# Kernel optimization log

Hardware: AMD Instinct MI355X
Metric: run time of the kernel (lower is better)

The kernel has to match this reference:

```python
import jax, jax.numpy as jnp
import numpy as np

E = 256   # in_features / embed_dim
O = 256   # out_features
H = 8     # n_heads
D = E // H  # head_dim
NEG = -1e9
SLOPE = 0.2  # leaky_relu negative slope


def setup_inputs() -> dict:
    key = jax.random.key(0)
    ks = jax.random.split(key, 9)
    B, N = 8, 1024
    x = jax.random.normal(ks[0], (B, N, E), dtype=jnp.float32)
    adj_matrix = jax.random.randint(ks[1], (N, N), 0, 2, dtype=jnp.int32)
    s = 1.0 / np.sqrt(E)
    w_in = jax.random.uniform(ks[2], (3 * E, E), jnp.float32, -s, s)   # packed q/k/v proj (torch in_proj_weight)
    b_in = jnp.zeros((3 * E,), jnp.float32)
    w_out = jax.random.uniform(ks[3], (E, E), jnp.float32, -s, s)      # MHA out_proj
    b_out = jnp.zeros((E,), jnp.float32)
    w_lin = jax.random.uniform(ks[4], (O, E), jnp.float32, -s, s)      # final nn.Linear
    b_lin = jax.random.uniform(ks[5], (O,), jnp.float32, -s, s)
    return {"x": x, "adj_matrix": adj_matrix, "w_in": w_in, "b_in": b_in,
            "w_out": w_out, "b_out": b_out, "w_lin": w_lin, "b_lin": b_lin}


def reference(x, adj_matrix, w_in, b_in, w_out, b_out, w_lin, b_lin):
    B, N, _ = x.shape
    scale = 1.0 / np.sqrt(D)
    qkv = x @ w_in.T + b_in                      # [B,N,3E]
    q, k, v = jnp.split(qkv, 3, axis=-1)
    q = q.reshape(B, N, H, D) * scale
    k = k.reshape(B, N, H, D)
    v = v.reshape(B, N, H, D)
    scores = jnp.einsum('bnhd,bmhd->bhnm', q, k)  # [B,H,N,N]
    allowed = (adj_matrix != 0)[None, None]       # mask True where adj==0 -> disallowed
    scores = jnp.where(allowed, scores, NEG)
    attn = jax.nn.softmax(scores, axis=-1)
    ctx = jnp.einsum('bhnm,bmhd->bnhd', attn, v).reshape(B, N, E)
    attended = ctx @ w_out.T + b_out              # MHA output (dropout is identity in eval)
    out = attended @ w_lin.T + b_lin
    return jnp.where(out >= 0, out, SLOPE * out)  # leaky_relu(0.2)
```

## Files before the change

### kernel.cpp

```cpp
#include <hip/hip_runtime.h>
#include <math.h>

#define EE 256
#define HH 8
#define DD 32
#define NB 8
#define NS 1024
#define SLOPE 0.2f

typedef float f32x4 __attribute__((ext_vector_type(4)));
typedef short short8 __attribute__((ext_vector_type(8)));

static __device__ __forceinline__ unsigned short f2b(float f) {
    unsigned int u = __float_as_uint(f);
    u = (u + 0x7FFFu + ((u >> 16) & 1u)) >> 16;
    return (unsigned short)u;
}

static __device__ __forceinline__ unsigned int cvtpk(float lo, float hi) {
    unsigned int r;
    asm("v_cvt_pk_bf16_f32 %0, %1, %2" : "=v"(r) : "v"(lo), "v"(hi));
    return r;
}

static __device__ __forceinline__ void gload_lds16(const void* g, void* l) {
    __builtin_amdgcn_global_load_lds(
        (const __attribute__((address_space(1))) unsigned int*)g,
        (__attribute__((address_space(3))) unsigned int*)l, 16, 0, 0);
}

__global__ __launch_bounds__(256) void cvt_w(
    const float* __restrict__ wi, const float* __restrict__ wo,
    const float* __restrict__ wl, unsigned short* __restrict__ wib,
    unsigned short* __restrict__ wob, unsigned short* __restrict__ wlb) {
    int t = blockIdx.x * 256 + threadIdx.x;
    const float* src; unsigned short* dst; int base;
    if (t < 24576)      { src = wi; dst = wib; base = t; }
    else if (t < 32768) { src = wo; dst = wob; base = t - 24576; }
    else                { src = wl; dst = wlb; base = t - 32768; }
    const float4* s = (const float4*)(src + (size_t)base * 8);
    float4 a = s[0], b = s[1];
    uint4 wv;
    wv.x = cvtpk(a.x, a.y); wv.y = cvtpk(a.z, a.w);
    wv.z = cvtpk(b.x, b.y); wv.w = cvtpk(b.z, b.w);
    *(uint4*)(dst + (size_t)base * 8) = wv;
}

__global__ __launch_bounds__(256) void adj_to_bits(const int* __restrict__ adj,
                                                   unsigned int* __restrict__ bits) {
    int t = blockIdx.x * 256 + threadIdx.x;
    int n = t >> 5, w = t & 31;
    const int* p = adj + (size_t)n * NS + w * 32;
    unsigned int word = 0;
#pragma unroll
    for (int i = 0; i < 32; i += 4) {
        int4 a = *(const int4*)(p + i);
        if (a.x) word |= 1u << i;
        if (a.y) word |= 1u << (i + 1);
        if (a.z) word |= 1u << (i + 2);
        if (a.w) word |= 1u << (i + 3);
    }
    bits[t] = word;
}

template<int MODE>
__global__ __launch_bounds__(256) void gemm_mfma(
    const unsigned short* __restrict__ A, const float* __restrict__ Af,
    const unsigned short* __restrict__ W,
    const float* __restrict__ bias, void* __restrict__ out,
    unsigned short* __restrict__ qb, unsigned short* __restrict__ kb,
    unsigned short* __restrict__ vtb, int Nout) {
    __shared__ __align__(16) unsigned short As[128 * 64];
    __shared__ __align__(16) unsigned short Bs[64 * 64];
    int tid = threadIdx.x, w = tid >> 6, lane = tid & 63;
    int lq = lane & 15, g = lane >> 4;
    int wr = w >> 1, wc = w & 1;
    int m0 = blockIdx.y * 128, n0 = blockIdx.x * 64;
    int r8 = lane >> 3, c8 = (lane & 7) * 8;
    f32x4 acc[4][2];
#pragma unroll
    for (int i = 0; i < 4; ++i)
#pragma unroll
        for (int j = 0; j < 2; ++j) acc[i][j] = (f32x4){0.f, 0.f, 0.f, 0.f};

    for (int k0 = 0; k0 < 256; k0 += 64) {
        __syncthreads();
        if (MODE == 2) {
#pragma unroll
            for (int u = 0; u < 4; ++u) {
                int idx = u * 256 + tid;
                int r = idx >> 3, cc = (idx & 7) * 8;
                const float* src = Af + (size_t)(m0 + r) * 256 + k0 + cc;
                float4 a = *(const float4*)src;
                float4 b = *(const float4*)(src + 4);
                uint4 wv;
                wv.x = cvtpk(a.x, a.y); wv.y = cvtpk(a.z, a.w);
                wv.z = cvtpk(b.x, b.y); wv.w = cvtpk(b.z, b.w);
                *(uint4*)(&As[r * 64 + cc]) = wv;
            }
        } else {
#pragma unroll
            for (int i = 0; i < 4; ++i)
                gload_lds16(A + (size_t)(m0 + w * 32 + i * 8 + r8) * 256 + k0 + c8,
                            &As[(w * 32 + i * 8) * 64]);
        }
#pragma unroll
        for (int i = 0; i < 2; ++i)
            gload_lds16(W + (size_t)(n0 + w * 16 + i * 8 + r8) * 256 + k0 + c8,
                        &Bs[(w * 16 + i * 8) * 64]);
        __syncthreads();
#pragma unroll
        for (int ks = 0; ks < 2; ++ks) {
            short8 af[4], bf[2];
#pragma unroll
            for (int mi = 0; mi < 4; ++mi)
                af[mi] = *(const short8*)(&As[(wr * 64 + mi * 16 + lq) * 64 + ks * 32 + g * 8]);
#pragma unroll
            for (int ni = 0; ni < 2; ++ni)
                bf[ni] = *(const short8*)(&Bs[(wc * 32 + ni * 16 + lq) * 64 + ks * 32 + g * 8]);
#pragma unroll
            for (int mi = 0; mi < 4; ++mi)
#pragma unroll
                for (int ni = 0; ni < 2; ++ni)
                    acc[mi][ni] = __builtin_amdgcn_mfma_f32_16x16x32_bf16(af[mi], bf[ni], acc[mi][ni], 0, 0, 0);
        }
    }
    const float scale = 0.17677669529663687f;
#pragma unroll
    for (int mi = 0; mi < 4; ++mi) {
#pragma unroll
        for (int reg = 0; reg < 4; ++reg) {
            int m = m0 + wr * 64 + mi * 16 + g * 4 + reg;
#pragma unroll
            for (int ni = 0; ni < 2; ++ni) {
                int n = n0 + wc * 32 + ni * 16 + lq;
                float v = acc[mi][ni][reg] + bias[n];
                if (MODE == 0) {
                    ((unsigned short*)out)[(size_t)m * Nout + n] = f2b(v);
                } else if (MODE == 1) {
                    v = v >= 0.f ? v : SLOPE * v;
                    ((float*)out)[(size_t)m * Nout + n] = v;
                } else {
                    int sec = n >> 8, cc = n & 255, h = cc >> 5, d = cc & 31;
                    int b = m >> 10, nr = m & (NS - 1);
                    if (sec == 0)
                        qb[((size_t)(b * HH + h) * NS + nr) * DD + d] = f2b(v * scale);
                    else if (sec == 1)
                        kb[((size_t)(b * HH + h) * NS + nr) * DD + d] = f2b(v);
                    else
                        vtb[((size_t)(b * HH + h) * DD + d) * NS + nr] = f2b(v);
                }
            }
        }
    }
}

__global__ __launch_bounds__(256) void attn_mfma(
    const unsigned short* __restrict__ q, const unsigned short* __restrict__ k,
    const unsigned short* __restrict__ vt, const unsigned int* __restrict__ adjbits,
    unsigned short* __restrict__ ctx) {
    __shared__ __align__(16) unsigned short Ks[128 * 40];
    __shared__ __align__(16) unsigned short Vs[32 * 136];
    __shared__ __align__(16) unsigned short Ps[4 * 16 * 136];
    int tid = threadIdx.x;
    int w = tid >> 6, lane = tid & 63;
    int lq = lane & 15, g = lane >> 4;
    int bh = blockIdx.y;
    int n0 = blockIdx.x * 64;
    int nq = n0 + w * 16 + lq;
    const unsigned short* qb = q + (size_t)bh * NS * DD;
    const unsigned short* kb = k + (size_t)bh * NS * DD;
    const unsigned short* vb = vt + (size_t)bh * DD * NS;
    short8 qfrag = *(const short8*)(qb + (size_t)nq * DD + g * 8);
    const unsigned int* abr = adjbits + (size_t)nq * 32;
    float ls[4] = {0.f, 0.f, 0.f, 0.f};
    f32x4 acc0 = {0.f, 0.f, 0.f, 0.f}, acc1 = {0.f, 0.f, 0.f, 0.f};
    unsigned short* Pw = Ps + w * 16 * 136;
    int kr = tid >> 1, kc = (tid & 1) * 16;
    int vd = tid >> 3, vc = (tid & 7) * 16;

    for (int m0 = 0; m0 < NS; m0 += 128) {
        __syncthreads();
        {
            const unsigned short* ksrc = kb + (size_t)(m0 + kr) * DD + kc;
            *(int4*)(&Ks[kr * 40 + kc])     = *(const int4*)(ksrc);
            *(int4*)(&Ks[kr * 40 + kc + 8]) = *(const int4*)(ksrc + 8);
            const unsigned short* vsrc = vb + (size_t)vd * NS + m0 + vc;
            *(int4*)(&Vs[vd * 136 + vc])     = *(const int4*)(vsrc);
            *(int4*)(&Vs[vd * 136 + vc + 8]) = *(const int4*)(vsrc + 8);
        }
        __syncthreads();

        const f32x4 z = {0.f, 0.f, 0.f, 0.f};
        f32x4 s[8];
#pragma unroll
        for (int t = 0; t < 8; ++t) {
            short8 kf = *(const short8*)(&Ks[(16 * t + lq) * 40 + g * 8]);
            s[t] = __builtin_amdgcn_mfma_f32_16x16x32_bf16(kf, qfrag, z, 0, 0, 0);
        }
        uint4 w4 = *(const uint4*)(abr + (m0 >> 5));
#pragma unroll
        for (int t = 0; t < 8; ++t) {
            unsigned int wd = (t < 2) ? w4.x : (t < 4) ? w4.y : (t < 6) ? w4.z : w4.w;
            unsigned int bits = wd >> (16 * (t & 1) + 4 * g);
            float p0 = ((bits >> 0) & 1u) ? __expf(s[t][0]) : 0.f;
            float p1 = ((bits >> 1) & 1u) ? __expf(s[t][1]) : 0.f;
            float p2 = ((bits >> 2) & 1u) ? __expf(s[t][2]) : 0.f;
            float p3 = ((bits >> 3) & 1u) ? __expf(s[t][3]) : 0.f;
            ls[0] += p0; ls[1] += p1; ls[2] += p2; ls[3] += p3;
            uint2 uu;
            uu.x = cvtpk(p0, p1);
            uu.y = cvtpk(p2, p3);
            *(uint2*)(&Pw[lq * 136 + 16 * t + 4 * g]) = uu;
        }
#pragma unroll
        for (int kh = 0; kh < 4; ++kh) {
            short8 pf = *(const short8*)(&Pw[lq * 136 + kh * 32 + g * 8]);
            short8 v0 = *(const short8*)(&Vs[lq * 136 + kh * 32 + g * 8]);
            short8 v1 = *(const short8*)(&Vs[(16 + lq) * 136 + kh * 32 + g * 8]);
            acc0 = __builtin_amdgcn_mfma_f32_16x16x32_bf16(pf, v0, acc0, 0, 0, 0);
            acc1 = __builtin_amdgcn_mfma_f32_16x16x32_bf16(pf, v1, acc1, 0, 0, 0);
        }
    }
    float rs = (ls[0] + ls[1]) + (ls[2] + ls[3]);
    rs += __shfl_xor(rs, 16);
    rs += __shfl_xor(rs, 32);
    int b = bh >> 3, h = bh & 7;
#pragma unroll
    for (int i = 0; i < 4; ++i) {
        int nrow = n0 + w * 16 + g * 4 + i;
        float inv = 1.f / __shfl(rs, g * 4 + i);
        unsigned short* dst = ctx + ((size_t)(b * NS + nrow)) * EE + h * DD;
        dst[lq] = f2b(acc0[i] * inv);
        dst[16 + lq] = f2b(acc1[i] * inv);
    }
}

extern "C" void kernel_launch(void* const* d_in, const int* in_sizes, int n_in,
                              void* d_out, int out_size, void* d_ws, size_t ws_size,
                              hipStream_t stream) {
    const float* x     = (const float*)d_in[0];
    const int*   adj   = (const int*)d_in[1];
    const float* w_in  = (const float*)d_in[2];
    const float* b_in  = (const float*)d_in[3];
    const float* w_out = (const float*)d_in[4];
    const float* b_out = (const float*)d_in[5];
    const float* w_lin = (const float*)d_in[6];
    const float* b_lin = (const float*)d_in[7];
    float* out = (float*)d_out;

    const size_t S = (size_t)NB * HH * NS * DD;
    unsigned short* qb   = (unsigned short*)d_ws;
    unsigned short* kb   = qb + S;
    unsigned short* vtb  = kb + S;
    unsigned short* ctxb = vtb + S;
    unsigned short* attb = ctxb + S;
    unsigned short* wib  = attb + S;
    unsigned short* wob  = wib + 768 * 256;
    unsigned short* wlb  = wob + 256 * 256;
    unsigned int* adjbits = (unsigned int*)(wlb + 256 * 256);

    dim3 blk(256);
    cvt_w<<<dim3(160), blk, 0, stream>>>(w_in, w_out, w_lin, wib, wob, wlb);
    adj_to_bits<<<dim3((NS * 32) / 256), blk, 0, stream>>>(adj, adjbits);
    gemm_mfma<2><<<dim3(12, 64), blk, 0, stream>>>(nullptr, x, wib, b_in, nullptr, qb, kb, vtb, 768);
    attn_mfma<<<dim3(NS / 64, NB * HH), blk, 0, stream>>>(qb, kb, vtb, adjbits, ctxb);
    gemm_mfma<0><<<dim3(4, 64), blk, 0, stream>>>(ctxb, nullptr, wob, b_out, attb, nullptr, nullptr, nullptr, 256);
    gemm_mfma<1><<<dim3(4, 64), blk, 0, stream>>>(attb, nullptr, wlb, b_lin, out, nullptr, nullptr, nullptr, 256);
}
```

Measured before the change: 79.14 us.

## Fold out_proj and final linear into one combined weight; pre-convert x to bf16

Precomputes W_lin·W_out and the combined bias on the device each call, so the two back-to-back linear layers become a single GEMM. This drops one GEMM launch and the bf16 round trip of the intermediate activations. The x-to-bf16 conversion also moves out of the QKV GEMM into its own pass, so that GEMM can use direct global-to-LDS loads. In exchange it adds a naive fp32 256x256x256 weight product kernel and extra launches, and rounds the combined weight to bf16.

```diff
diff --git a/kernel.cpp b/kernel.cpp
--- a/kernel.cpp
+++ b/kernel.cpp
@@ -29,21 +29,44 @@
         (__attribute__((address_space(3))) unsigned int*)l, 16, 0, 0);
 }
 
-__global__ __launch_bounds__(256) void cvt_w(
-    const float* __restrict__ wi, const float* __restrict__ wo,
-    const float* __restrict__ wl, unsigned short* __restrict__ wib,
-    unsigned short* __restrict__ wob, unsigned short* __restrict__ wlb) {
+__global__ __launch_bounds__(256) void cvt_x(const float* __restrict__ x,
+                                             unsigned short* __restrict__ xb) {
     int t = blockIdx.x * 256 + threadIdx.x;
-    const float* src; unsigned short* dst; int base;
-    if (t < 24576)      { src = wi; dst = wib; base = t; }
-    else if (t < 32768) { src = wo; dst = wob; base = t - 24576; }
-    else                { src = wl; dst = wlb; base = t - 32768; }
-    const float4* s = (const float4*)(src + (size_t)base * 8);
+    const float4* s = (const float4*)(x + (size_t)t * 8);
     float4 a = s[0], b = s[1];
     uint4 wv;
     wv.x = cvtpk(a.x, a.y); wv.y = cvtpk(a.z, a.w);
     wv.z = cvtpk(b.x, b.y); wv.w = cvtpk(b.z, b.w);
-    *(uint4*)(dst + (size_t)base * 8) = wv;
+    *(uint4*)(xb + (size_t)t * 8) = wv;
+}
+
+__global__ __launch_bounds__(256) void cvt_wi(const float* __restrict__ wi,
+                                              unsigned short* __restrict__ wib) {
+    int t = blockIdx.x * 256 + threadIdx.x;
+    const float4* s = (const float4*)(wi + (size_t)t * 8);
+    float4 a = s[0], b = s[1];
+    uint4 wv;
+    wv.x = cvtpk(a.x, a.y); wv.y = cvtpk(a.z, a.w);
+    wv.z = cvtpk(b.x, b.y); wv.w = cvtpk(b.z, b.w);
+    *(uint4*)(wib + (size_t)t * 8) = wv;
+}
+
+__global__ __launch_bounds__(256) void make_comb(
+    const float* __restrict__ wo, const float* __restrict__ bo,
+    const float* __restrict__ wl, const float* __restrict__ bl,
+    unsigned short* __restrict__ wcb, float* __restrict__ bcomb) {
+    int o = blockIdx.x, c = threadIdx.x;
+    const float* wlr = wl + (size_t)o * EE;
+    float acc = 0.f;
+#pragma unroll 8
+    for (int e = 0; e < EE; ++e)
+        acc = fmaf(wlr[e], wo[(size_t)e * EE + c], acc);
+    wcb[(size_t)o * EE + c] = f2b(acc);
+    if (c == 0) {
+        float bb = bl[o];
+        for (int e = 0; e < EE; ++e) bb = fmaf(wlr[e], bo[e], bb);
+        bcomb[o] = bb;
+    }
 }
 
 __global__ __launch_bounds__(256) void adj_to_bits(const int* __restrict__ adj,
@@ -65,8 +88,7 @@
 
 template<int MODE>
 __global__ __launch_bounds__(256) void gemm_mfma(
-    const unsigned short* __restrict__ A, const float* __restrict__ Af,
-    const unsigned short* __restrict__ W,
+    const unsigned short* __restrict__ A, const unsigned short* __restrict__ W,
     const float* __restrict__ bias, void* __restrict__ out,
     unsigned short* __restrict__ qb, unsigned short* __restrict__ kb,
     unsigned short* __restrict__ vtb, int Nout) {
@@ -85,25 +107,10 @@
 
     for (int k0 = 0; k0 < 256; k0 += 64) {
         __syncthreads();
-        if (MODE == 2) {
-#pragma unroll
-            for (int u = 0; u < 4; ++u) {
-                int idx = u * 256 + tid;
-                int r = idx >> 3, cc = (idx & 7) * 8;
-                const float* src = Af + (size_t)(m0 + r) * 256 + k0 + cc;
-                float4 a = *(const float4*)src;
-                float4 b = *(const float4*)(src + 4);
-                uint4 wv;
-                wv.x = cvtpk(a.x, a.y); wv.y = cvtpk(a.z, a.w);
-                wv.z = cvtpk(b.x, b.y); wv.w = cvtpk(b.z, b.w);
-                *(uint4*)(&As[r * 64 + cc]) = wv;
-            }
-        } else {
-#pragma unroll
-            for (int i = 0; i < 4; ++i)
-                gload_lds16(A + (size_t)(m0 + w * 32 + i * 8 + r8) * 256 + k0 + c8,
-                            &As[(w * 32 + i * 8) * 64]);
-        }
+#pragma unroll
+        for (int i = 0; i < 4; ++i)
+            gload_lds16(A + (size_t)(m0 + w * 32 + i * 8 + r8) * 256 + k0 + c8,
+                        &As[(w * 32 + i * 8) * 64]);
 #pragma unroll
         for (int i = 0; i < 2; ++i)
             gload_lds16(W + (size_t)(n0 + w * 16 + i * 8 + r8) * 256 + k0 + c8,
@@ -135,9 +142,7 @@
             for (int ni = 0; ni < 2; ++ni) {
                 int n = n0 + wc * 32 + ni * 16 + lq;
                 float v = acc[mi][ni][reg] + bias[n];
-                if (MODE == 0) {
-                    ((unsigned short*)out)[(size_t)m * Nout + n] = f2b(v);
-                } else if (MODE == 1) {
+                if (MODE == 1) {
                     v = v >= 0.f ? v : SLOPE * v;
                     ((float*)out)[(size_t)m * Nout + n] = v;
                 } else {
@@ -254,17 +259,18 @@
     unsigned short* kb   = qb + S;
     unsigned short* vtb  = kb + S;
     unsigned short* ctxb = vtb + S;
-    unsigned short* attb = ctxb + S;
-    unsigned short* wib  = attb + S;
-    unsigned short* wob  = wib + 768 * 256;
-    unsigned short* wlb  = wob + 256 * 256;
-    unsigned int* adjbits = (unsigned int*)(wlb + 256 * 256);
+    unsigned short* xb   = ctxb + S;
+    unsigned short* wib  = xb + S;
+    unsigned short* wcb  = wib + 768 * 256;
+    unsigned int* adjbits = (unsigned int*)(wcb + 256 * 256);
+    float* bcomb = (float*)(adjbits + 32768);
 
     dim3 blk(256);
-    cvt_w<<<dim3(160), blk, 0, stream>>>(w_in, w_out, w_lin, wib, wob, wlb);
+    cvt_x<<<dim3(1024), blk, 0, stream>>>(x, xb);
+    cvt_wi<<<dim3(96), blk, 0, stream>>>(w_in, wib);
+    make_comb<<<dim3(256), blk, 0, stream>>>(w_out, b_out, w_lin, b_lin, wcb, bcomb);
     adj_to_bits<<<dim3((NS * 32) / 256), blk, 0, stream>>>(adj, adjbits);
-    gemm_mfma<2><<<dim3(12, 64), blk, 0, stream>>>(nullptr, x, wib, b_in, nullptr, qb, kb, vtb, 768);
+    gemm_mfma<2><<<dim3(12, 64), blk, 0, stream>>>(xb, wib, b_in, nullptr, qb, kb, vtb, 768);
     attn_mfma<<<dim3(NS / 64, NB * HH), blk, 0, stream>>>(qb, kb, vtb, adjbits, ctxb);
-    gemm_mfma<0><<<dim3(4, 64), blk, 0, stream>>>(ctxb, nullptr, wob, b_out, attb, nullptr, nullptr, nullptr, 256);
-    gemm_mfma<1><<<dim3(4, 64), blk, 0, stream>>>(attb, nullptr, wlb, b_lin, out, nullptr, nullptr, nullptr, 256);
-}
+    gemm_mfma<1><<<dim3(4, 64), blk, 0, stream>>>(ctxb, wcb, bcomb, out, nullptr, nullptr, nullptr, 256);
+}
```

Measured after the change: 85.35 us. +7.8%, slower.
